# Optimization experiments

Measured on AMD Instinct MI355X. Metric: run time of the kernel, lower is better.

The kernel has to match this reference:

```python
import jax, jax.numpy as jnp
import numpy as np

N_FFT = 4096
HOP = 1024
WIN = 4096
DIAG_EPS = 1e-7
EPS = 1e-8

# asteroid-style periodic sqrt-hann analysis/synthesis window
_n = np.arange(WIN)
WINDOW = jnp.asarray(np.sqrt(0.5 - 0.5 * np.cos(2.0 * np.pi * _n / WIN)), dtype=jnp.float32)


def _frame_idx(n_samp):
    T = (n_samp - WIN) // HOP + 1
    return np.arange(T)[:, None] * HOP + np.arange(WIN)[None, :]


def stft(x):
    """x: (..., N) -> (real, imag) each (..., F, T) with F = N_FFT//2+1."""
    idx = _frame_idx(x.shape[-1])
    frames = x[..., idx] * WINDOW
    spec = jnp.fft.rfft(frames, axis=-1)     # (..., T, F) complex64
    spec = jnp.moveaxis(spec, -2, -1)        # (..., F, T)
    return spec.real, spec.imag


def istft(re, im, out_len):
    """(..., F, T) -> (..., out_len) via windowed overlap-add."""
    spec = jnp.moveaxis(re + 1j * im, -1, -2)            # (..., T, F)
    frames = jnp.fft.irfft(spec, n=WIN, axis=-1) * WINDOW
    T = frames.shape[-2]
    full = (T - 1) * HOP + WIN
    idx = _frame_idx(full).reshape(-1)
    flat = frames.reshape(frames.shape[:-2] + (-1,))
    out = jnp.zeros(frames.shape[:-2] + (full,), frames.dtype).at[..., idx].add(flat)
    wsq = jnp.zeros((full,), jnp.float32).at[idx].add(jnp.tile(WINDOW ** 2, T))
    out = out / jnp.maximum(wsq, 1e-8)
    return out[..., :out_len]


def psd_causal(re, im):
    """Causal, frame-normalized PSD. re/im: (B, C, F, T) -> complex (B, T, F, C, C)."""
    pr = jnp.einsum('saft,sbft->sabft', re, re) + jnp.einsum('saft,sbft->sabft', im, im)
    pi = jnp.einsum('saft,sbft->sbaft', re, im) - jnp.einsum('saft,sbft->sabft', re, im)
    cnt = jnp.arange(1, re.shape[-1] + 1, dtype=re.dtype)
    pr = jnp.cumsum(pr, -1) / cnt
    pi = jnp.cumsum(pi, -1) / cnt
    psd = pr + 1j * pi                       # (B, a, b, F, T)
    return jnp.transpose(psd, (0, 4, 3, 1, 2))  # (B, T, F, C, C)


def mvdr_vector(psd_s, psd_n):
    """Souden MVDR: ws = inv(Npsd) @ Spsd / (tr(.) + eps). (..., C, C) complex."""
    C = psd_n.shape[-1]
    tr_n = jnp.trace(psd_n, axis1=-2, axis2=-1).real
    epsilon = jax.lax.stop_gradient(tr_n * DIAG_EPS + EPS)
    psd_n = psd_n + epsilon[..., None, None] * jnp.eye(C, dtype=psd_n.dtype)
    num = jnp.linalg.inv(psd_n) @ psd_s
    return num / (jnp.trace(num, axis1=-2, axis2=-1)[..., None, None] + EPS)


def _forward(x, s):
    B, S, C, N = s.shape
    xs = jnp.broadcast_to(x[:, None], (B, S, C, N)).reshape(B * S, C, N)
    ss = s.reshape(B * S, C, N)
    Xr, Xi = stft(xs)
    Sr, Si = stft(ss)
    Nr, Ni = Xr - Sr, Xi - Si
    Sscm = psd_causal(Sr, Si)   # (BS, T, F, C, C)
    Nscm = psd_causal(Nr, Ni)
    ws = mvdr_vector(Sscm, Nscm)  # (BS, T, F, C, C)
    # conj(filter), rearranged to (BS, a, b, F, T)
    fr = jnp.transpose(ws.real, (0, 3, 4, 2, 1))
    fi = -jnp.transpose(ws.imag, (0, 3, 4, 2, 1))
    enh_r = jnp.einsum('sabft,saft->sbft', fr, Xr) - jnp.einsum('sabft,saft->sbft', fi, Xi)
    enh_i = jnp.einsum('sabft,saft->sbft', fr, Xi) + jnp.einsum('sabft,saft->sbft', fi, Xr)
    est = istft(enh_r, enh_i, N)            # (BS, C, N)
    return est.reshape(B, S, C, N)


def setup_inputs() -> dict:
    key = jax.random.key(0)
    kx, ks = jax.random.split(key)
    x = jax.random.normal(kx, (2, 4, 32768), dtype=jnp.float32)
    s = jax.random.normal(ks, (2, 2, 4, 32768), dtype=jnp.float32)
    return {"x": x, "s": s, "do_permute": 0}


def reference(x, s, do_permute):
    # do_permute=False path (PIT permutation is a data-dependent preprocessing step)
    return _forward(x, s)
```

## Files before the change

### kernel.cpp

```cpp
#include <hip/hip_runtime.h>

static constexpr int NFFT = 4096;
static constexpr int HOP  = 1024;
static constexpr int NF   = 2049;
static constexpr int NT   = 29;
static constexpr int NS   = 32768;
static constexpr int NB   = 2;
static constexpr int NSrc = 2;
static constexpr int NC   = 4;
static constexpr int NBS  = NB * NSrc;
static constexpr int FCHUNKS = (NF + 7) / 8;

#define PI_F     3.14159265358979323846f
#define TWO_PI_F 6.28318530717958647692f

#define IDX(a) ((a) + ((a) >> 4))
static constexpr int LDSN = 2048 + 128;

__device__ inline float2 cmul(float2 a, float2 b) {
    return make_float2(a.x * b.x - a.y * b.y, a.x * b.y + a.y * b.x);
}
__device__ inline float2 cmulc(float2 a, float2 b) {
    return make_float2(a.x * b.x + a.y * b.y, a.y * b.x - a.x * b.y);
}

template <int CTRL, int RMASK>
__device__ __forceinline__ float dpp0(float x) {
    return __int_as_float(__builtin_amdgcn_update_dpp(
        0, __float_as_int(x), CTRL, RMASK, 0xF, true));
}

template <int DIR>
__device__ inline void fft4v(float2 v[4]) {
    float2 t0 = make_float2(v[0].x + v[2].x, v[0].y + v[2].y);
    float2 t1 = make_float2(v[0].x - v[2].x, v[0].y - v[2].y);
    float2 t2 = make_float2(v[1].x + v[3].x, v[1].y + v[3].y);
    float2 t3 = make_float2(v[1].x - v[3].x, v[1].y - v[3].y);
    v[0] = make_float2(t0.x + t2.x, t0.y + t2.y);
    v[2] = make_float2(t0.x - t2.x, t0.y - t2.y);
    if (DIR < 0) {
        v[1] = make_float2(t1.x + t3.y, t1.y - t3.x);
        v[3] = make_float2(t1.x - t3.y, t1.y + t3.x);
    } else {
        v[1] = make_float2(t1.x - t3.y, t1.y + t3.x);
        v[3] = make_float2(t1.x + t3.y, t1.y - t3.x);
    }
}

template <int DIR>
__device__ inline void fft8v(float2 v[8]) {
    float2 e[4] = { v[0], v[2], v[4], v[6] };
    float2 o[4] = { v[1], v[3], v[5], v[7] };
    fft4v<DIR>(e);
    fft4v<DIR>(o);
    const float c = 0.70710678118654752f;
    float2 o0 = o[0], o1, o2, o3;
    if (DIR < 0) {
        o1 = make_float2(c * (o[1].x + o[1].y), c * (o[1].y - o[1].x));
        o2 = make_float2(o[2].y, -o[2].x);
        o3 = make_float2(c * (o[3].y - o[3].x), -c * (o[3].x + o[3].y));
    } else {
        o1 = make_float2(c * (o[1].x - o[1].y), c * (o[1].y + o[1].x));
        o2 = make_float2(-o[2].y, o[2].x);
        o3 = make_float2(-c * (o[3].x + o[3].y), c * (o[3].x - o[3].y));
    }
    v[0] = make_float2(e[0].x + o0.x, e[0].y + o0.y);
    v[4] = make_float2(e[0].x - o0.x, e[0].y - o0.y);
    v[1] = make_float2(e[1].x + o1.x, e[1].y + o1.y);
    v[5] = make_float2(e[1].x - o1.x, e[1].y - o1.y);
    v[2] = make_float2(e[2].x + o2.x, e[2].y + o2.y);
    v[6] = make_float2(e[2].x - o2.x, e[2].y - o2.y);
    v[3] = make_float2(e[3].x + o3.x, e[3].y + o3.y);
    v[7] = make_float2(e[3].x - o3.x, e[3].y - o3.y);
}

template <int DIR, int NSs>
__device__ inline void stage8(const float* __restrict__ reS, const float* __restrict__ imS,
                              float* __restrict__ reD, float* __restrict__ imD, int tid) {
    int j = tid;
    float2 v[8];
    #pragma unroll
    for (int r = 0; r < 8; ++r) {
        int a = IDX(j + (r << 8));
        v[r] = make_float2(reS[a], imS[a]);
    }
    if (NSs > 1) {
        float ang = (float)DIR * (TWO_PI_F / (8.0f * (float)NSs)) * (float)(j & (NSs - 1));
        float2 w1; __sincosf(ang, &w1.y, &w1.x);
        float2 w = w1;
        v[1] = cmul(v[1], w);
        #pragma unroll
        for (int r = 2; r < 8; ++r) { w = cmul(w, w1); v[r] = cmul(v[r], w); }
    }
    fft8v<DIR>(v);
    int idxD = ((j & ~(NSs - 1)) << 3) + (j & (NSs - 1));
    #pragma unroll
    for (int r = 0; r < 8; ++r) {
        int a = IDX(idxD + r * NSs);
        reD[a] = v[r].x;
        imD[a] = v[r].y;
    }
}

template <int DIR>
__device__ inline void stage4_512(const float* __restrict__ reS, const float* __restrict__ imS,
                                  float* __restrict__ reD, float* __restrict__ imD, int tid) {
    #pragma unroll
    for (int h = 0; h < 2; ++h) {
        int j = tid + (h << 8);
        float2 v[4];
        #pragma unroll
        for (int r = 0; r < 4; ++r) {
            int a = IDX(j + (r << 9));
            v[r] = make_float2(reS[a], imS[a]);
        }
        float ang = (float)DIR * (TWO_PI_F / 2048.0f) * (float)j;
        float2 w1; __sincosf(ang, &w1.y, &w1.x);
        float2 w2 = cmul(w1, w1);
        float2 w3 = cmul(w2, w1);
        v[1] = cmul(v[1], w1);
        v[2] = cmul(v[2], w2);
        v[3] = cmul(v[3], w3);
        fft4v<DIR>(v);
        #pragma unroll
        for (int r = 0; r < 4; ++r) {
            int a = IDX(j + (r << 9));
            reD[a] = v[r].x;
            imD[a] = v[r].y;
        }
    }
}

template <int DIR>
__device__ inline void fft2048(float* reA, float* imA, float* reB, float* imB, int tid) {
    stage8<DIR, 1>(reA, imA, reB, imB, tid);  __syncthreads();
    stage8<DIR, 8>(reB, imB, reA, imA, tid);  __syncthreads();
    stage8<DIR, 64>(reA, imA, reB, imB, tid); __syncthreads();
    stage4_512<DIR>(reB, imB, reA, imA, tid); __syncthreads();
}

__global__ __launch_bounds__(256) void stft_kernel(
    const float* __restrict__ x, const float* __restrict__ s,
    float2* __restrict__ Xs, float2* __restrict__ Ss) {
    __shared__ float reA[LDSN], imA[LDSN], reB[LDSN], imB[LDSN];
    int tid = threadIdx.x;
    int fid = blockIdx.x;
    const float* src;
    float2* dst;
    if (fid < NB * NC * NT) {
        int b = fid / (NC * NT);
        int r = fid % (NC * NT);
        int c = r / NT;
        int t = r % NT;
        src = x + (size_t)((b * NC + c) * NS + t * HOP);
        dst = Xs + (size_t)((b * NC + c) * NT + t) * NF;
    } else {
        int g  = fid - NB * NC * NT;
        int bs = g / (NC * NT);
        int r  = g % (NC * NT);
        int c  = r / NT;
        int t  = r % NT;
        src = s + (size_t)((bs * NC + c) * NS + t * HOP);
        dst = Ss + (size_t)((bs * NC + c) * NT + t) * NF;
    }
    const float2* s2 = (const float2*)src;
    for (int n = tid; n < 2048; n += 256) {
        float2 v = s2[n];
        float we = __sinf((float)n * (PI_F / 2048.0f));
        float wo = __sinf((float)(2 * n + 1) * (PI_F / 4096.0f));
        int a = IDX(n);
        reA[a] = v.x * we;
        imA[a] = v.y * wo;
    }
    __syncthreads();
    fft2048<-1>(reA, imA, reB, imB, tid);
    for (int k = tid; k <= 1024; k += 256) {
        int a1 = IDX(k);
        int a2 = IDX((2048 - k) & 2047);
        float2 Za = make_float2(reA[a1], imA[a1]);
        float2 Zb = make_float2(reA[a2], imA[a2]);
        if (k == 0) {
            dst[0]    = make_float2(Za.x + Za.y, 0.f);
            dst[2048] = make_float2(Za.x - Za.y, 0.f);
        } else {
            float2 Ze = make_float2(0.5f * (Za.x + Zb.x),  0.5f * (Za.y - Zb.y));
            float2 Zo = make_float2(0.5f * (Za.y + Zb.y), -0.5f * (Za.x - Zb.x));
            float ang = -(PI_F / 2048.0f) * (float)k;
            float2 W; __sincosf(ang, &W.y, &W.x);
            float2 WZo = cmul(W, Zo);
            dst[k] = make_float2(Ze.x + WZo.x, Ze.y + WZo.y);
            if (k < 1024)
                dst[2048 - k] = make_float2(Ze.x - WZo.x, -(Ze.y - WZo.y));
        }
    }
}

__global__ __launch_bounds__(256, 1) void mvdr2_kernel(
    const float2* __restrict__ Xs, const float2* __restrict__ Ss,
    float2* __restrict__ Es) {
    __shared__ float2 ldsS[4][32][9];
    __shared__ float2 ldsX[4][32][9];
    int tid = threadIdx.x;
    int blk = blockIdx.x;
    int bs  = blk / FCHUNKS;
    int f0  = (blk % FCHUNKS) * 8;
    int b   = bs >> 1;

    for (int idx = tid; idx < 2048; idx += 256) {
        int fi = idx & 7;
        int tt = (idx >> 3) & 31;
        int q  = idx >> 8;
        int c  = q & 3;
        int f  = f0 + fi;
        float2 val = make_float2(0.f, 0.f);
        if (tt < NT && f < NF) {
            val = (q >= 4) ? Xs[(size_t)((b  * NC + c) * NT + tt) * NF + f]
                           : Ss[(size_t)((bs * NC + c) * NT + tt) * NF + f];
        }
        if (q >= 4) ldsX[c][tt][fi] = val; else ldsS[c][tt][fi] = val;
    }
    __syncthreads();

    int lane  = tid & 63;
    int wave  = tid >> 6;
    int t     = lane & 31;
    int fpair = lane >> 5;
    int fi    = wave * 2 + fpair;

    float2 Sv[4], Xv[4], Nv[4];
    #pragma unroll
    for (int c = 0; c < 4; ++c) {
        Sv[c] = ldsS[c][t][fi];
        Xv[c] = ldsX[c][t][fi];
        Nv[c] = make_float2(Xv[c].x - Sv[c].x, Xv[c].y - Sv[c].y);
    }

    float v[32];
    #pragma unroll
    for (int c = 0; c < 4; ++c) {
        v[c]      = Sv[c].x * Sv[c].x + Sv[c].y * Sv[c].y;
        v[16 + c] = Nv[c].x * Nv[c].x + Nv[c].y * Nv[c].y;
    }
    constexpr int PI6[6] = {0, 0, 0, 1, 1, 2};
    constexpr int PJ6[6] = {1, 2, 3, 2, 3, 3};
    #pragma unroll
    for (int p = 0; p < 6; ++p) {
        float2 d = cmulc(Sv[PI6[p]], Sv[PJ6[p]]);
        v[4 + 2 * p] = d.x; v[5 + 2 * p] = d.y;
        d = cmulc(Nv[PI6[p]], Nv[PJ6[p]]);
        v[20 + 2 * p] = d.x; v[21 + 2 * p] = d.y;
    }

    #pragma unroll
    for (int k = 0; k < 32; ++k) v[k] += dpp0<0x111, 0xF>(v[k]);
    #pragma unroll
    for (int k = 0; k < 32; ++k) v[k] += dpp0<0x112, 0xF>(v[k]);
    #pragma unroll
    for (int k = 0; k < 32; ++k) v[k] += dpp0<0x114, 0xF>(v[k]);
    #pragma unroll
    for (int k = 0; k < 32; ++k) v[k] += dpp0<0x118, 0xF>(v[k]);
    #pragma unroll
    for (int k = 0; k < 32; ++k) v[k] += dpp0<0x142, 0xA>(v[k]);

    float ic = 1.0f / (float)(t + 1);
    float2 ps[4][4];
    float2 M[4][8];
    #pragma unroll
    for (int c = 0; c < 4; ++c) {
        ps[c][c]   = make_float2(v[c] * ic, 0.f);
        M[c][c]    = make_float2(v[16 + c] * ic, 0.f);
        #pragma unroll
        for (int j = 0; j < 4; ++j)
            M[c][4 + j] = make_float2((c == j) ? 1.f : 0.f, 0.f);
    }
    #pragma unroll
    for (int p = 0; p < 6; ++p) {
        int i = PI6[p], j = PJ6[p];
        float re = v[4 + 2 * p] * ic, im = v[5 + 2 * p] * ic;
        ps[i][j] = make_float2(re, im);
        ps[j][i] = make_float2(re, -im);
        re = v[20 + 2 * p] * ic; im = v[21 + 2 * p] * ic;
        M[i][j] = make_float2(re, im);
        M[j][i] = make_float2(re, -im);
    }

    float eps = (M[0][0].x + M[1][1].x + M[2][2].x + M[3][3].x) * 1e-7f + 1e-8f;
    #pragma unroll
    for (int i = 0; i < 4; ++i) M[i][i].x += eps;

    #pragma unroll
    for (int col = 0; col < 4; ++col) {
        float2 piv = M[col][col];
        float  idd = 1.0f / (piv.x * piv.x + piv.y * piv.y);
        float2 pinv = make_float2(piv.x * idd, -piv.y * idd);
        #pragma unroll
        for (int j = col + 1; j < 8; ++j) M[col][j] = cmul(M[col][j], pinv);
        #pragma unroll
        for (int rr = 0; rr < 4; ++rr) {
            if (rr == col) continue;
            float2 fac = M[rr][col];
            #pragma unroll
            for (int j = col + 1; j < 8; ++j) {
                float2 d = cmul(fac, M[col][j]);
                M[rr][j].x -= d.x; M[rr][j].y -= d.y;
            }
        }
    }

    float2 z[4];
    #pragma unroll
    for (int k = 0; k < 4; ++k) {
        float2 acc = make_float2(0.f, 0.f);
        #pragma unroll
        for (int a = 0; a < 4; ++a) {
            float2 q = M[a][4 + k];
            acc.x += q.x * Xv[a].x + q.y * Xv[a].y;
            acc.y += q.x * Xv[a].y - q.y * Xv[a].x;
        }
        z[k] = acc;
    }

    float2 trc = make_float2(1e-8f, 0.f);
    #pragma unroll
    for (int i = 0; i < 4; ++i)
        #pragma unroll
        for (int k = 0; k < 4; ++k) {
            float2 q = M[i][4 + k];
            float2 p = ps[k][i];
            trc.x += q.x * p.x - q.y * p.y;
            trc.y += q.x * p.y + q.y * p.x;
        }
    float ginv = 1.0f / (trc.x * trc.x + trc.y * trc.y);
    float2 g = make_float2(trc.x * ginv, trc.y * ginv);

    #pragma unroll
    for (int bo = 0; bo < 4; ++bo) {
        float2 u = make_float2(0.f, 0.f);
        #pragma unroll
        for (int k = 0; k < 4; ++k) {
            float2 d = cmul(ps[bo][k], z[k]);
            u.x += d.x; u.y += d.y;
        }
        ldsS[bo][t][fi] = cmul(g, u);
    }
    __syncthreads();

    for (int idx = tid; idx < 1024; idx += 256) {
        int fi2 = idx & 7;
        int tt  = (idx >> 3) & 31;
        int bo  = idx >> 8;
        int ff  = f0 + fi2;
        if (tt < NT && ff < NF)
            Es[(size_t)((bs * NC + bo) * NT + tt) * NF + ff] = ldsS[bo][tt][fi2];
    }
}

__global__ __launch_bounds__(256) void istft_kernel(
    const float2* __restrict__ Es, float* __restrict__ Fr) {
    __shared__ float reA[LDSN], imA[LDSN], reB[LDSN], imB[LDSN];
    int tid = threadIdx.x;
    int fid = blockIdx.x;
    int bs = fid / (NC * NT);
    int r  = fid % (NC * NT);
    int c  = r / NT;
    int t  = r % NT;
    const float2* src = Es + (size_t)((bs * NC + c) * NT + t) * NF;
    for (int k = tid; k <= 1024; k += 256) {
        float2 A = src[k];
        float2 B = src[2048 - k];
        float2 Ze = make_float2(0.5f * (A.x + B.x), 0.5f * (A.y - B.y));
        float2 D  = make_float2(0.5f * (A.x - B.x), 0.5f * (A.y + B.y));
        float ang = (PI_F / 2048.0f) * (float)k;
        float2 W; __sincosf(ang, &W.y, &W.x);
        float2 Zo = cmul(W, D);
        int a1 = IDX(k);
        reA[a1] = Ze.x - Zo.y;
        imA[a1] = Ze.y + Zo.x;
        if (k > 0 && k < 1024) {
            int a2 = IDX(2048 - k);
            reA[a2] = Ze.x + Zo.y;
            imA[a2] = -Ze.y + Zo.x;
        }
    }
    __syncthreads();
    fft2048<1>(reA, imA, reB, imB, tid);
    float2* d2 = (float2*)(Fr + (size_t)((bs * NC + c) * NT + t) * NFFT);
    for (int n = tid; n < 2048; n += 256) {
        int a = IDX(n);
        float we = __sinf((float)n * (PI_F / 2048.0f)) * (1.0f / 2048.0f);
        float wo = __sinf((float)(2 * n + 1) * (PI_F / 4096.0f)) * (1.0f / 2048.0f);
        d2[n] = make_float2(reA[a] * we, imA[a] * wo);
    }
}

__global__ __launch_bounds__(256) void ola_kernel(
    const float* __restrict__ Fr, float* __restrict__ out) {
    int idx = blockIdx.x * 256 + threadIdx.x;
    const int total = NBS * NC * NS;
    if (idx >= total) return;
    int p  = idx & (NS - 1);
    int ch = idx >> 15;
    int t1 = p >> 10;
    if (t1 > NT - 1) t1 = NT - 1;
    int t0 = (p >= NFFT) ? ((p - (NFFT - 1) + (HOP - 1)) >> 10) : 0;
    float acc = 0.f, wacc = 0.f;
    for (int t = t0; t <= t1; ++t) {
        int   j = p - (t << 10);
        float w = __sinf((float)j * (PI_F / 4096.0f));
        acc  += Fr[((size_t)(ch * NT + t) << 12) + j];
        wacc += w * w;
    }
    out[idx] = acc / fmaxf(wacc, 1e-8f);
}

extern "C" void kernel_launch(void* const* d_in, const int* in_sizes, int n_in,
                              void* d_out, int out_size, void* d_ws, size_t ws_size,
                              hipStream_t stream) {
    const float* x = (const float*)d_in[0];
    const float* s = (const float*)d_in[1];
    float* out = (float*)d_out;

    const size_t XS_N = (size_t)NB  * NC * NT * NF;
    const size_t SS_N = (size_t)NBS * NC * NT * NF;
    float2* Xs = (float2*)d_ws;
    float2* Ss = Xs + XS_N;
    float2* Es = Ss + SS_N;
    float*  Fr = (float*)(Es + SS_N);

    stft_kernel<<<NB * NC * NT + NBS * NC * NT, 256, 0, stream>>>(x, s, Xs, Ss);

    mvdr2_kernel<<<NBS * FCHUNKS, 256, 0, stream>>>(Xs, Ss, Es);

    istft_kernel<<<NBS * NC * NT, 256, 0, stream>>>(Es, Fr);

    int ola_total = NBS * NC * NS;
    ola_kernel<<<(ola_total + 255) / 256, 256, 0, stream>>>(Fr, out);
}
```

Baseline: 43.76 us.

## Replace Gauss-Jordan inverse with Hermitian LDL^H solve and real trace

Replaces the per-bin complex Gauss-Jordan inversion of the 4x4 noise PSD with an LDL^H factorization. It uses the matrix's Hermitian structure, forward/back substitution for the filtered vector, and a real-valued trace computed as a quadratic form through the explicit inverse-L factors. The 1/(t+1) normalisation cancels in the Souden ratio, so it is dropped and the epsilon is rescaled to match. It also switches to fast hardware reciprocals. This cuts ALU work and register pressure in the MVDR stage, at the cost of slightly different numerics (approximate rcp, no pivoting).

```diff
diff --git a/kernel.cpp b/kernel.cpp
--- a/kernel.cpp
+++ b/kernel.cpp
@@ -262,87 +262,125 @@
     #pragma unroll
     for (int k = 0; k < 32; ++k) v[k] += dpp0<0x142, 0xA>(v[k]);
 
-    float ic = 1.0f / (float)(t + 1);
-    float2 ps[4][4];
-    float2 M[4][8];
-    #pragma unroll
-    for (int c = 0; c < 4; ++c) {
-        ps[c][c]   = make_float2(v[c] * ic, 0.f);
-        M[c][c]    = make_float2(v[16 + c] * ic, 0.f);
-        #pragma unroll
-        for (int j = 0; j < 4; ++j)
-            M[c][4 + j] = make_float2((c == j) ? 1.f : 0.f, 0.f);
-    }
-    #pragma unroll
-    for (int p = 0; p < 6; ++p) {
-        int i = PI6[p], j = PJ6[p];
-        float re = v[4 + 2 * p] * ic, im = v[5 + 2 * p] * ic;
-        ps[i][j] = make_float2(re, im);
-        ps[j][i] = make_float2(re, -im);
-        re = v[20 + 2 * p] * ic; im = v[21 + 2 * p] * ic;
-        M[i][j] = make_float2(re, im);
-        M[j][i] = make_float2(re, -im);
-    }
-
-    float eps = (M[0][0].x + M[1][1].x + M[2][2].x + M[3][3].x) * 1e-7f + 1e-8f;
-    #pragma unroll
-    for (int i = 0; i < 4; ++i) M[i][i].x += eps;
-
-    #pragma unroll
-    for (int col = 0; col < 4; ++col) {
-        float2 piv = M[col][col];
-        float  idd = 1.0f / (piv.x * piv.x + piv.y * piv.y);
-        float2 pinv = make_float2(piv.x * idd, -piv.y * idd);
-        #pragma unroll
-        for (int j = col + 1; j < 8; ++j) M[col][j] = cmul(M[col][j], pinv);
-        #pragma unroll
-        for (int rr = 0; rr < 4; ++rr) {
-            if (rr == col) continue;
-            float2 fac = M[rr][col];
-            #pragma unroll
-            for (int j = col + 1; j < 8; ++j) {
-                float2 d = cmul(fac, M[col][j]);
-                M[rr][j].x -= d.x; M[rr][j].y -= d.y;
-            }
-        }
-    }
-
-    float2 z[4];
-    #pragma unroll
-    for (int k = 0; k < 4; ++k) {
-        float2 acc = make_float2(0.f, 0.f);
-        #pragma unroll
-        for (int a = 0; a < 4; ++a) {
-            float2 q = M[a][4 + k];
-            acc.x += q.x * Xv[a].x + q.y * Xv[a].y;
-            acc.y += q.x * Xv[a].y - q.y * Xv[a].x;
-        }
-        z[k] = acc;
-    }
-
-    float2 trc = make_float2(1e-8f, 0.f);
-    #pragma unroll
-    for (int i = 0; i < 4; ++i)
-        #pragma unroll
-        for (int k = 0; k < 4; ++k) {
-            float2 q = M[i][4 + k];
-            float2 p = ps[k][i];
-            trc.x += q.x * p.x - q.y * p.y;
-            trc.y += q.x * p.y + q.y * p.x;
-        }
-    float ginv = 1.0f / (trc.x * trc.x + trc.y * trc.y);
-    float2 g = make_float2(trc.x * ginv, trc.y * ginv);
-
-    #pragma unroll
-    for (int bo = 0; bo < 4; ++bo) {
-        float2 u = make_float2(0.f, 0.f);
-        #pragma unroll
-        for (int k = 0; k < 4; ++k) {
-            float2 d = cmul(ps[bo][k], z[k]);
-            u.x += d.x; u.y += d.y;
-        }
-        ldsS[bo][t][fi] = cmul(g, u);
-    }
+    float pd0 = v[0], pd1 = v[1], pd2 = v[2], pd3 = v[3];
+    float2 po0 = make_float2(v[4],  v[5]);
+    float2 po1 = make_float2(v[6],  v[7]);
+    float2 po2 = make_float2(v[8],  v[9]);
+    float2 po3 = make_float2(v[10], v[11]);
+    float2 po4 = make_float2(v[12], v[13]);
+    float2 po5 = make_float2(v[14], v[15]);
+    float eps = (v[16] + v[17] + v[18] + v[19]) * 1e-7f + (float)(t + 1) * 1e-8f;
+    float nd0 = v[16] + eps, nd1 = v[17] + eps, nd2 = v[18] + eps, nd3 = v[19] + eps;
+    float2 no0 = make_float2(v[20], v[21]);
+    float2 no1 = make_float2(v[22], v[23]);
+    float2 no2 = make_float2(v[24], v[25]);
+    float2 no3 = make_float2(v[26], v[27]);
+    float2 no4 = make_float2(v[28], v[29]);
+    float2 no5 = make_float2(v[30], v[31]);
+
+    float D0 = nd0;
+    float r0 = __builtin_amdgcn_rcpf(D0);
+    float2 L10 = make_float2(no0.x * r0, -no0.y * r0);
+    float2 L20 = make_float2(no1.x * r0, -no1.y * r0);
+    float2 L30 = make_float2(no2.x * r0, -no2.y * r0);
+    float D1 = nd1 - (L10.x * L10.x + L10.y * L10.y) * D0;
+    float r1 = __builtin_amdgcn_rcpf(D1);
+    float2 c10 = make_float2(D0 * L10.x, -D0 * L10.y);
+    float2 tA = cmul(L20, c10);
+    float2 L21 = make_float2((no3.x - tA.x) * r1, (-no3.y - tA.y) * r1);
+    float2 tB = cmul(L30, c10);
+    float2 L31 = make_float2((no4.x - tB.x) * r1, (-no4.y - tB.y) * r1);
+    float D2 = nd2 - (L20.x * L20.x + L20.y * L20.y) * D0
+                   - (L21.x * L21.x + L21.y * L21.y) * D1;
+    float r2 = __builtin_amdgcn_rcpf(D2);
+    float2 c20 = make_float2(D0 * L20.x, -D0 * L20.y);
+    float2 c21 = make_float2(D1 * L21.x, -D1 * L21.y);
+    float2 tC = cmul(L30, c20);
+    float2 tD = cmul(L31, c21);
+    float2 L32 = make_float2((no5.x - tC.x - tD.x) * r2, (-no5.y - tC.y - tD.y) * r2);
+    float D3 = nd3 - (L30.x * L30.x + L30.y * L30.y) * D0
+                   - (L31.x * L31.x + L31.y * L31.y) * D1
+                   - (L32.x * L32.x + L32.y * L32.y) * D2;
+    float r3 = __builtin_amdgcn_rcpf(D3);
+
+    float2 u0 = Xv[0];
+    float2 m0 = cmul(L10, u0);
+    float2 u1 = make_float2(Xv[1].x - m0.x, Xv[1].y - m0.y);
+    float2 m1 = cmul(L20, u0), m2 = cmul(L21, u1);
+    float2 u2 = make_float2(Xv[2].x - m1.x - m2.x, Xv[2].y - m1.y - m2.y);
+    float2 m3 = cmul(L30, u0), m4 = cmul(L31, u1), m5 = cmul(L32, u2);
+    float2 u3 = make_float2(Xv[3].x - m3.x - m4.x - m5.x,
+                            Xv[3].y - m3.y - m4.y - m5.y);
+    float2 w0 = make_float2(u0.x * r0, u0.y * r0);
+    float2 w1 = make_float2(u1.x * r1, u1.y * r1);
+    float2 w2 = make_float2(u2.x * r2, u2.y * r2);
+    float2 w3 = make_float2(u3.x * r3, u3.y * r3);
+    float2 z3 = w3;
+    float2 n0_ = cmulc(z3, L32);
+    float2 z2 = make_float2(w2.x - n0_.x, w2.y - n0_.y);
+    float2 n1_ = cmulc(z2, L21), n2_ = cmulc(z3, L31);
+    float2 z1 = make_float2(w1.x - n1_.x - n2_.x, w1.y - n1_.y - n2_.y);
+    float2 n3_ = cmulc(z1, L10), n4_ = cmulc(z2, L20), n5_ = cmulc(z3, L30);
+    float2 z0 = make_float2(w0.x - n3_.x - n4_.x - n5_.x,
+                            w0.y - n3_.y - n4_.y - n5_.y);
+
+    float2 K10 = make_float2(-L10.x, -L10.y);
+    float2 kk  = cmul(L21, L10);
+    float2 K20 = make_float2(kk.x - L20.x, kk.y - L20.y);
+    float2 K21 = make_float2(-L21.x, -L21.y);
+    kk = cmul(L32, L21);
+    float2 K31 = make_float2(kk.x - L31.x, kk.y - L31.y);
+    float2 K32 = make_float2(-L32.x, -L32.y);
+    float2 ka = cmul(K31, L10), kb = cmul(L32, L20);
+    float2 K30 = make_float2(-L30.x - ka.x + kb.x, -L30.y - ka.y + kb.y);
+
+    float q0 = pd0;
+    float2 qm = cmul(K10, po0);
+    float q1 = pd1 + (K10.x * K10.x + K10.y * K10.y) * pd0 + 2.0f * qm.x;
+    qm = cmul(K20, po0);
+    float s_a = qm.x * K21.x + qm.y * K21.y;
+    qm = cmul(K20, po1);
+    float s_b = qm.x;
+    qm = cmul(K21, po3);
+    float s_c = qm.x;
+    float q2 = pd2 + (K20.x * K20.x + K20.y * K20.y) * pd0
+                   + (K21.x * K21.x + K21.y * K21.y) * pd1
+                   + 2.0f * (s_a + s_b + s_c);
+    qm = cmul(K30, po0);
+    float s1 = qm.x * K31.x + qm.y * K31.y;
+    qm = cmul(K30, po1);
+    float s2 = qm.x * K32.x + qm.y * K32.y;
+    qm = cmul(K30, po2);
+    float s3 = qm.x;
+    qm = cmul(K31, po3);
+    float s4 = qm.x * K32.x + qm.y * K32.y;
+    qm = cmul(K31, po4);
+    float s5 = qm.x;
+    qm = cmul(K32, po5);
+    float s6 = qm.x;
+    float q3 = pd3 + (K30.x * K30.x + K30.y * K30.y) * pd0
+                   + (K31.x * K31.x + K31.y * K31.y) * pd1
+                   + (K32.x * K32.x + K32.y * K32.y) * pd2
+                   + 2.0f * (s1 + s2 + s3 + s4 + s5 + s6);
+    float tr = q0 * r0 + q1 * r1 + q2 * r2 + q3 * r3;
+    float g  = __builtin_amdgcn_rcpf(tr + 1e-8f);
+
+    float2 a0 = cmul(po0, z1), a1 = cmul(po1, z2), a2 = cmul(po2, z3);
+    float2 e0 = make_float2(pd0 * z0.x + a0.x + a1.x + a2.x,
+                            pd0 * z0.y + a0.y + a1.y + a2.y);
+    a0 = cmulc(z0, po0); a1 = cmul(po3, z2); a2 = cmul(po4, z3);
+    float2 e1 = make_float2(a0.x + pd1 * z1.x + a1.x + a2.x,
+                            a0.y + pd1 * z1.y + a1.y + a2.y);
+    a0 = cmulc(z0, po1); a1 = cmulc(z1, po3); a2 = cmul(po5, z3);
+    float2 e2 = make_float2(a0.x + a1.x + pd2 * z2.x + a2.x,
+                            a0.y + a1.y + pd2 * z2.y + a2.y);
+    a0 = cmulc(z0, po2); a1 = cmulc(z1, po4); a2 = cmulc(z2, po5);
+    float2 e3 = make_float2(a0.x + a1.x + a2.x + pd3 * z3.x,
+                            a0.y + a1.y + a2.y + pd3 * z3.y);
+    ldsS[0][t][fi] = make_float2(e0.x * g, e0.y * g);
+    ldsS[1][t][fi] = make_float2(e1.x * g, e1.y * g);
+    ldsS[2][t][fi] = make_float2(e2.x * g, e2.y * g);
+    ldsS[3][t][fi] = make_float2(e3.x * g, e3.y * g);
     __syncthreads();
 
     for (int idx = tid; idx < 1024; idx += 256) {
```

Result: faster. 39.39 us (-10.0%).
